# Kernel tuning notes

Measured on AMD Instinct MI355X. Metric: run time of the kernel, lower is better.

Reference implementation:

```python
import jax, jax.numpy as jnp
import numpy as np

FIELD_NUM = 24

def _pair_indices(f):
    ii, jj = np.triu_indices(f, k=1)
    return jnp.asarray(ii), jnp.asarray(jj)

def setup_inputs() -> dict:
    key = jax.random.key(0)
    k1, k2 = jax.random.split(key)
    B, F, D = 16384, FIELD_NUM, 64
    P = F * (F - 1) // 2  # 276
    x = jax.random.normal(k1, (B, F, D), dtype=jnp.float32)
    W = jax.random.normal(k2, (P, D, D), dtype=jnp.float32) * 0.05
    return {"x": x, "W": W}

def reference(x, W):
    # x: (B, F, D) field embeddings; W: (P, D, D) per-pair bilinear matrices
    idx_i, idx_j = _pair_indices(FIELD_NUM)
    xi = x[:, idx_i, :]  # (B, P, D)
    xj = x[:, idx_j, :]  # (B, P, D)
    # sum_{p,d,e} xi[b,p,d] * W[p,d,e] * xj[b,p,e]
    logit = jnp.einsum('bpd,pde,bpe->b', xi, W, xj)
    return logit[:, None]  # (B, 1), matching tf output shape
```

## Files before the change

kernel.cpp:

```cpp
#include <hip/hip_runtime.h>
#include <stdint.h>

#define B_TOT 16384
#define F_NUM 24
#define P_NUM 276
#define BT    32
#define NTH   1024
#define ROWP  1544

typedef float f32x16 __attribute__((ext_vector_type(16)));
typedef short bf16x8 __attribute__((ext_vector_type(8)));

__device__ inline unsigned short f2bf(float f) {
    unsigned u = __float_as_uint(f);
    u += 0x7fffu + ((u >> 16) & 1u);
    return (unsigned short)(u >> 16);
}
__device__ inline float bf2f(unsigned short h) {
    return __uint_as_float(((unsigned)h) << 16);
}

struct Tab { int ent[16][18]; int cnt[16]; };
constexpr Tab build_tab() {
    Tab t{};
    int ii[276] = {}, jj[276] = {};
    int n = 0;
    for (int i = 0; i < 24; ++i)
        for (int j = i + 1; j < 24; ++j) { ii[n] = i; jj[n] = j; ++n; }
    int pos = 0;
    for (int w = 0; w < 16; ++w) {
        int c = (w < 4) ? 18 : 17;
        t.cnt[w] = c;
        for (int k = 0; k < c; ++k, ++pos) {
            int flag = (k == c - 1) || (ii[pos + 1] != ii[pos]);
            t.ent[w][k] = pos | (jj[pos] << 9) | (ii[pos] << 14) | (flag << 19);
        }
    }
    return t;
}
__device__ __constant__ Tab gtab = build_tab();

__global__ __launch_bounds__(256) void wprep(const float* __restrict__ W,
                                             unsigned short* __restrict__ afrag) {
    __shared__ __align__(16) unsigned short wlds[64 * 72];
    int p = blockIdx.x, t = threadIdx.x;
    const float4* src = (const float4*)(W + (size_t)p * 4096);
    #pragma unroll
    for (int c = 0; c < 4; ++c) {
        int i = t + c * 256;
        float4 v = src[i];
        int d = i >> 4;
        int e = (i & 15) * 4;
        ushort4 h; h.x=f2bf(v.x); h.y=f2bf(v.y); h.z=f2bf(v.z); h.w=f2bf(v.w);
        *(ushort4*)(&wlds[d * 72 + e]) = h;
    }
    __syncthreads();
    #pragma unroll
    for (int c = 0; c < 2; ++c) {
        int sl = t + c * 256;
        int u = sl >> 6, lane = sl & 63;
        int ks = u >> 1, m = u & 1;
        int d = m * 32 + (lane & 31);
        int e = ks * 16 + (lane >> 5) * 8;
        bf16x8 v = *(const bf16x8*)(&wlds[d * 72 + e]);
        *(bf16x8*)(afrag + ((size_t)(p * 8 + u) * 64 + lane) * 8) = v;
    }
}

#define LDA4(P_, HALF_, A0,A1,A2,A3) do {                                      \
    const bf16x8* ap_ = afr + (size_t)(P_) * 512 + (HALF_) * 256 + lane;       \
    A0 = ap_[0]; A1 = ap_[64]; A2 = ap_[128]; A3 = ap_[192]; } while (0)

#define HSTEP(E_, NP_, HALF_, A0,A1,A2,A3) do {                                \
    int jb_ = ((E_ >> 9) & 31) * 64 + q8 + (HALF_) * 32;                       \
    const unsigned short* bp_ = xrow + jb_;                                    \
    bf16x8 bt0_ = *(const bf16x8*)(bp_);                                       \
    bf16x8 bt1_ = *(const bf16x8*)(bp_ + 16);                                  \
    a0 = __builtin_amdgcn_mfma_f32_32x32x16_bf16(A0, bt0_, a0, 0, 0, 0);       \
    a1 = __builtin_amdgcn_mfma_f32_32x32x16_bf16(A1, bt0_, a1, 0, 0, 0);       \
    a0 = __builtin_amdgcn_mfma_f32_32x32x16_bf16(A2, bt1_, a0, 0, 0, 0);       \
    a1 = __builtin_amdgcn_mfma_f32_32x32x16_bf16(A3, bt1_, a1, 0, 0, 0);       \
    LDA4(NP_, HALF_, A0,A1,A2,A3); } while (0)

__global__ __launch_bounds__(NTH, 4) void fmfm_main(const float* __restrict__ x,
                                                    const unsigned short* __restrict__ afrag,
                                                    float* __restrict__ out) {
    __shared__ __align__(16) unsigned short xs[BT * ROWP];
    __shared__ float t_red[BT];
    const int tid = threadIdx.x;
    const int btile = blockIdx.x;
    const int lane = tid & 63;
    const int wv = __builtin_amdgcn_readfirstlane(tid >> 6);
    const int bcol = lane & 31;
    const int q = lane >> 5;
    const int q8 = q * 8, q4 = q * 4;

    if (tid < BT) t_red[tid] = 0.0f;

    const bf16x8* afr = (const bf16x8*)afrag;
    const unsigned short* xrow = xs + bcol * ROWP;

    float tacc = 0.f;
    f32x16 a0, a1;
    #pragma unroll
    for (int k = 0; k < 16; ++k) { a0[k] = 0.f; a1[k] = 0.f; }

    bf16x8 A0,A1,A2,A3;
    bf16x8 B0,B1,B2,B3;

    const int cnt = gtab.cnt[wv];
    {
        int p0 = gtab.ent[wv][0] & 511;
        LDA4(p0, 0, A0,A1,A2,A3);
        LDA4(p0, 1, B0,B1,B2,B3);
    }

    const float* xg = x + (size_t)btile * BT * 1536;
    #pragma unroll 4
    for (int c = 0; c < 12; ++c) {
        int idx = tid + c * NTH;
        int row = idx / 384;
        int c4  = idx - row * 384;
        float4 v = *(const float4*)(xg + (size_t)row * 1536 + c4 * 4);
        ushort4 h; h.x=f2bf(v.x); h.y=f2bf(v.y); h.z=f2bf(v.z); h.w=f2bf(v.w);
        *(ushort4*)(&xs[row * ROWP + c4 * 4]) = h;
    }
    __syncthreads();

    #pragma unroll 1
    for (int s = 0; s < cnt; ++s) {
        int e  = gtab.ent[wv][s];
        int sn = (s + 1 < cnt) ? s + 1 : s;
        int np = gtab.ent[wv][sn] & 511;
        HSTEP(e, np, 0, A0,A1,A2,A3);
        HSTEP(e, np, 1, B0,B1,B2,B3);
        if (e & (1 << 19)) {
            int fi = (e >> 14) & 31;
            const unsigned short* ep = xrow + fi * 64 + q4;
            #pragma unroll
            for (int g = 0; g < 4; ++g) {
                ushort4 u0 = *(const ushort4*)(ep + 8 * g);
                tacc += a0[4*g+0]*bf2f(u0.x) + a0[4*g+1]*bf2f(u0.y)
                      + a0[4*g+2]*bf2f(u0.z) + a0[4*g+3]*bf2f(u0.w);
                u0 = *(const ushort4*)(ep + 32 + 8 * g);
                tacc += a1[4*g+0]*bf2f(u0.x) + a1[4*g+1]*bf2f(u0.y)
                      + a1[4*g+2]*bf2f(u0.z) + a1[4*g+3]*bf2f(u0.w);
            }
            #pragma unroll
            for (int k = 0; k < 16; ++k) { a0[k] = 0.f; a1[k] = 0.f; }
        }
    }

    atomicAdd(&t_red[bcol], tacc);
    __syncthreads();
    if (tid < BT) out[(size_t)btile * BT + tid] = t_red[tid];
}

extern "C" void kernel_launch(void* const* d_in, const int* in_sizes, int n_in,
                              void* d_out, int out_size, void* d_ws, size_t ws_size,
                              hipStream_t stream) {
    const float* x = (const float*)d_in[0];
    const float* W = (const float*)d_in[1];
    float* out = (float*)d_out;
    unsigned short* afrag = (unsigned short*)d_ws;
    wprep<<<P_NUM, 256, 0, stream>>>(W, afrag);
    fmfm_main<<<B_TOT / BT, NTH, 0, stream>>>(x, afrag, out);
}
```

Baseline: 190.0 us.

## Triple-buffer W fragment prefetch across three pairs per loop iteration

Restructures the main loop to process three pairs per iteration, with three register sets holding full 64x64 W fragments prefetched three pairs ahead instead of one. The pair distribution is rebalanced so every wave's count is a multiple of three (12 waves take 18 pairs, 4 take 15). The goal is to hide global/L2 latency of the W fragment loads behind more MFMA work. The cost is three times the prefetch register footprint, which may cause spills or lower occupancy under the 1024-thread launch bound, and an uneven per-wave workload.

```diff
diff --git a/kernel.cpp b/kernel.cpp
--- a/kernel.cpp
+++ b/kernel.cpp
@@ -29,7 +29,7 @@
         for (int j = i + 1; j < 24; ++j) { ii[n] = i; jj[n] = j; ++n; }
     int pos = 0;
     for (int w = 0; w < 16; ++w) {
-        int c = (w < 4) ? 18 : 17;
+        int c = (w < 12) ? 18 : 15;
         t.cnt[w] = c;
         for (int k = 0; k < c; ++k, ++pos) {
             int flag = (k == c - 1) || (ii[pos + 1] != ii[pos]);
@@ -67,20 +67,42 @@
     }
 }
 
-#define LDA4(P_, HALF_, A0,A1,A2,A3) do {                                      \
-    const bf16x8* ap_ = afr + (size_t)(P_) * 512 + (HALF_) * 256 + lane;       \
-    A0 = ap_[0]; A1 = ap_[64]; A2 = ap_[128]; A3 = ap_[192]; } while (0)
+#define LDA8(P_, A0,A1,A2,A3,A4,A5,A6,A7) do {                                 \
+    const bf16x8* ap_ = afr + (size_t)(P_) * 512 + lane;                       \
+    A0 = ap_[0];   A1 = ap_[64];  A2 = ap_[128]; A3 = ap_[192];                \
+    A4 = ap_[256]; A5 = ap_[320]; A6 = ap_[384]; A7 = ap_[448]; } while (0)
 
-#define HSTEP(E_, NP_, HALF_, A0,A1,A2,A3) do {                                \
-    int jb_ = ((E_ >> 9) & 31) * 64 + q8 + (HALF_) * 32;                       \
+#define STEP(E_, NP_, A0,A1,A2,A3,A4,A5,A6,A7) do {                            \
+    int jb_ = ((E_ >> 9) & 31) * 64 + q8;                                      \
     const unsigned short* bp_ = xrow + jb_;                                    \
     bf16x8 bt0_ = *(const bf16x8*)(bp_);                                       \
     bf16x8 bt1_ = *(const bf16x8*)(bp_ + 16);                                  \
+    bf16x8 bt2_ = *(const bf16x8*)(bp_ + 32);                                  \
+    bf16x8 bt3_ = *(const bf16x8*)(bp_ + 48);                                  \
     a0 = __builtin_amdgcn_mfma_f32_32x32x16_bf16(A0, bt0_, a0, 0, 0, 0);       \
     a1 = __builtin_amdgcn_mfma_f32_32x32x16_bf16(A1, bt0_, a1, 0, 0, 0);       \
     a0 = __builtin_amdgcn_mfma_f32_32x32x16_bf16(A2, bt1_, a0, 0, 0, 0);       \
     a1 = __builtin_amdgcn_mfma_f32_32x32x16_bf16(A3, bt1_, a1, 0, 0, 0);       \
-    LDA4(NP_, HALF_, A0,A1,A2,A3); } while (0)
+    a0 = __builtin_amdgcn_mfma_f32_32x32x16_bf16(A4, bt2_, a0, 0, 0, 0);       \
+    a1 = __builtin_amdgcn_mfma_f32_32x32x16_bf16(A5, bt2_, a1, 0, 0, 0);       \
+    a0 = __builtin_amdgcn_mfma_f32_32x32x16_bf16(A6, bt3_, a0, 0, 0, 0);       \
+    a1 = __builtin_amdgcn_mfma_f32_32x32x16_bf16(A7, bt3_, a1, 0, 0, 0);       \
+    LDA8(NP_, A0,A1,A2,A3,A4,A5,A6,A7);                                        \
+    if (E_ & (1 << 19)) {                                                      \
+        int fi_ = (E_ >> 14) & 31;                                             \
+        const unsigned short* ep_ = xrow + fi_ * 64 + q4;                      \
+        _Pragma("unroll")                                                      \
+        for (int g = 0; g < 4; ++g) {                                          \
+            ushort4 u0 = *(const ushort4*)(ep_ + 8 * g);                       \
+            tacc += a0[4*g+0]*bf2f(u0.x) + a0[4*g+1]*bf2f(u0.y)                \
+                  + a0[4*g+2]*bf2f(u0.z) + a0[4*g+3]*bf2f(u0.w);               \
+            u0 = *(const ushort4*)(ep_ + 32 + 8 * g);                          \
+            tacc += a1[4*g+0]*bf2f(u0.x) + a1[4*g+1]*bf2f(u0.y)                \
+                  + a1[4*g+2]*bf2f(u0.z) + a1[4*g+3]*bf2f(u0.w);               \
+        }                                                                      \
+        _Pragma("unroll")                                                      \
+        for (int k = 0; k < 16; ++k) { a0[k] = 0.f; a1[k] = 0.f; }             \
+    } } while (0)
 
 __global__ __launch_bounds__(NTH, 4) void fmfm_main(const float* __restrict__ x,
                                                     const unsigned short* __restrict__ afrag,
@@ -105,15 +127,14 @@
     #pragma unroll
     for (int k = 0; k < 16; ++k) { a0[k] = 0.f; a1[k] = 0.f; }
 
-    bf16x8 A0,A1,A2,A3;
-    bf16x8 B0,B1,B2,B3;
+    bf16x8 PA0,PA1,PA2,PA3,PA4,PA5,PA6,PA7;
+    bf16x8 PB0,PB1,PB2,PB3,PB4,PB5,PB6,PB7;
+    bf16x8 PC0,PC1,PC2,PC3,PC4,PC5,PC6,PC7;
 
     const int cnt = gtab.cnt[wv];
-    {
-        int p0 = gtab.ent[wv][0] & 511;
-        LDA4(p0, 0, A0,A1,A2,A3);
-        LDA4(p0, 1, B0,B1,B2,B3);
-    }
+    LDA8(gtab.ent[wv][0] & 511, PA0,PA1,PA2,PA3,PA4,PA5,PA6,PA7);
+    LDA8(gtab.ent[wv][1] & 511, PB0,PB1,PB2,PB3,PB4,PB5,PB6,PB7);
+    LDA8(gtab.ent[wv][2] & 511, PC0,PC1,PC2,PC3,PC4,PC5,PC6,PC7);
 
     const float* xg = x + (size_t)btile * BT * 1536;
     #pragma unroll 4
@@ -128,27 +149,16 @@
     __syncthreads();
 
     #pragma unroll 1
-    for (int s = 0; s < cnt; ++s) {
-        int e  = gtab.ent[wv][s];
-        int sn = (s + 1 < cnt) ? s + 1 : s;
-        int np = gtab.ent[wv][sn] & 511;
-        HSTEP(e, np, 0, A0,A1,A2,A3);
-        HSTEP(e, np, 1, B0,B1,B2,B3);
-        if (e & (1 << 19)) {
-            int fi = (e >> 14) & 31;
-            const unsigned short* ep = xrow + fi * 64 + q4;
-            #pragma unroll
-            for (int g = 0; g < 4; ++g) {
-                ushort4 u0 = *(const ushort4*)(ep + 8 * g);
-                tacc += a0[4*g+0]*bf2f(u0.x) + a0[4*g+1]*bf2f(u0.y)
-                      + a0[4*g+2]*bf2f(u0.z) + a0[4*g+3]*bf2f(u0.w);
-                u0 = *(const ushort4*)(ep + 32 + 8 * g);
-                tacc += a1[4*g+0]*bf2f(u0.x) + a1[4*g+1]*bf2f(u0.y)
-                      + a1[4*g+2]*bf2f(u0.z) + a1[4*g+3]*bf2f(u0.w);
-            }
-            #pragma unroll
-            for (int k = 0; k < 16; ++k) { a0[k] = 0.f; a1[k] = 0.f; }
-        }
+    for (int s = 0; s < cnt; s += 3) {
+        int e0 = gtab.ent[wv][s];
+        int e1 = gtab.ent[wv][s + 1];
+        int e2 = gtab.ent[wv][s + 2];
+        int n0 = gtab.ent[wv][(s + 3 < cnt) ? s + 3 : cnt - 1] & 511;
+        int n1 = gtab.ent[wv][(s + 4 < cnt) ? s + 4 : cnt - 1] & 511;
+        int n2 = gtab.ent[wv][(s + 5 < cnt) ? s + 5 : cnt - 1] & 511;
+        STEP(e0, n0, PA0,PA1,PA2,PA3,PA4,PA5,PA6,PA7);
+        STEP(e1, n1, PB0,PB1,PB2,PB3,PB4,PB5,PB6,PB7);
+        STEP(e2, n2, PC0,PC1,PC2,PC3,PC4,PC5,PC6,PC7);
     }
 
     atomicAdd(&t_red[bcol], tacc);
```

New measurement: 289.2 us. 52.2% more time.
